# Optimization experiments

Hardware: AMD Instinct MI355X
Metric: run time of the kernel (lower is better)

Reference implementation:

```python
import jax, jax.numpy as jnp
import numpy as np

N0, N1, N2 = 128000, 256000, 128000  # total nodes/edges/triangles across batch
B = 64        # graphs per batch (equal-size graphs: 2000/4000/2000 simplices each)
F = 32        # input feature dim per simplex level
P = 2         # polynomial power in SCConv
OUT = 32      # SCConv output dims
KN, KE, KT = 30, 60, 30  # sort-pool k's
DC = F + OUT  # concat dim (orig_features=True) == conv1d kernel/stride
CO = 16       # conv1d out channels


def spmm(rows, cols, vals, X, n_rows):
    # y = A @ X for sparse A given in COO form (gather + segment-sum scatter)
    return jax.ops.segment_sum(vals[:, None] * X[cols], rows, num_segments=n_rows)


def sortpool(Xc, b, k):
    # per-graph: sort rows by last feature column (descending), keep top k
    n = Xc.shape[0] // b
    Xb = Xc.reshape(b, n, Xc.shape[1])
    _, idx = jax.lax.top_k(Xb[:, :, -1], k)
    return jnp.take_along_axis(Xb, idx[:, :, None], axis=1)  # [b, k, d]


def conv1d(x, w, stride):
    return jax.lax.conv_general_dilated(x, w, (stride,), 'VALID',
                                        dimension_numbers=('NCH', 'OIH', 'NCH'))


def setup_inputs() -> dict:
    key = jax.random.key(0)
    ks = iter(jax.random.split(key, 64))
    d = {}

    def add_sp(name, nnz, nr, nc):
        d[name + '_rows'] = jax.random.randint(next(ks), (nnz,), 0, nr, dtype=jnp.int32)
        d[name + '_cols'] = jax.random.randint(next(ks), (nnz,), 0, nc, dtype=jnp.int32)
        d[name + '_vals'] = jax.random.normal(next(ks), (nnz,), jnp.float32) * 0.1

    add_sp('L0', 8 * N0, N0, N0)
    add_sp('L1', 8 * N1, N1, N1)
    add_sp('L2', 8 * N2, N2, N2)
    add_sp('D1invB1', 2 * N1, N0, N1)
    add_sp('D2B1TD1inv', 2 * N1, N1, N0)
    add_sp('B2TD2inv', 3 * N2, N2, N1)
    add_sp('B2D3', 3 * N2, N1, N2)
    d['X0'] = jax.random.normal(next(ks), (N0, F), jnp.float32)
    d['X1'] = jax.random.normal(next(ks), (N1, F), jnp.float32)
    d['X2'] = jax.random.normal(next(ks), (N2, F), jnp.float32)
    for w in ['W_n2n', 'W_n2e', 'W_e2e', 'W_e2n', 'W_e2t', 'W_t2e', 'W_t2t']:
        d[w] = jax.random.normal(next(ks), (F * P, OUT), jnp.float32) * 0.05
    d['conv_w_nodes'] = jax.random.normal(next(ks), (CO, 1, DC), jnp.float32) * 0.05
    d['conv_w_edges'] = jax.random.normal(next(ks), (CO, 1, DC), jnp.float32) * 0.05
    d['conv_w_tri'] = jax.random.normal(next(ks), (CO, 1, DC), jnp.float32) * 0.05
    mlp_in = CO * (KN + KE + KT)  # 1920
    d['mlp_w1'] = jax.random.normal(next(ks), (mlp_in, 128), jnp.float32) * 0.05
    d['mlp_w_out'] = jax.random.normal(next(ks), (128, 2), jnp.float32) * 0.05
    d['batch_size'] = B
    return d


def reference(L0_rows, L0_cols, L0_vals, L1_rows, L1_cols, L1_vals,
              L2_rows, L2_cols, L2_vals,
              D1invB1_rows, D1invB1_cols, D1invB1_vals,
              D2B1TD1inv_rows, D2B1TD1inv_cols, D2B1TD1inv_vals,
              B2TD2inv_rows, B2TD2inv_cols, B2TD2inv_vals,
              B2D3_rows, B2D3_cols, B2D3_vals,
              X0, X1, X2,
              W_n2n, W_n2e, W_e2e, W_e2n, W_e2t, W_t2e, W_t2t,
              conv_w_nodes, conv_w_edges, conv_w_tri,
              mlp_w1, mlp_w_out, batch_size):
    # SCConv: polynomial feature lift (p=2) -> linear -> sparse aggregation
    X0p = jnp.concatenate([X0, X0 * X0], axis=1)  # [N0, 2F]
    X1p = jnp.concatenate([X1, X1 * X1], axis=1)
    X2p = jnp.concatenate([X2, X2 * X2], axis=1)
    n2n = spmm(L0_rows, L0_cols, L0_vals, X0p @ W_n2n, N0)
    n2e = spmm(D2B1TD1inv_rows, D2B1TD1inv_cols, D2B1TD1inv_vals, X0p @ W_n2e, N1)
    e2n = spmm(D1invB1_rows, D1invB1_cols, D1invB1_vals, X1p @ W_e2n, N0)
    e2e = spmm(L1_rows, L1_cols, L1_vals, X1p @ W_e2e, N1)
    e2t = spmm(B2TD2inv_rows, B2TD2inv_cols, B2TD2inv_vals, X1p @ W_e2t, N2)
    t2t = spmm(L2_rows, L2_cols, L2_vals, X2p @ W_t2t, N2)
    t2e = spmm(B2D3_rows, B2D3_cols, B2D3_vals, X2p @ W_t2e, N1)
    X0o = 0.5 * jax.nn.relu(n2n + e2n)
    X1o = (1.0 / 3.0) * jax.nn.relu(e2e + n2e + t2e)
    X2o = 0.5 * jax.nn.relu(t2t + e2t)
    # orig_features=True: concat input features with conv output
    X0c = jnp.concatenate([X0, X0o], axis=1)  # [N0, DC]
    X1c = jnp.concatenate([X1, X1o], axis=1)
    X2c = jnp.concatenate([X2, X2o], axis=1)
    b = batch_size
    # sort-pool -> flatten -> 1D conv (kernel=stride=DC, no bias) -> relu
    nodes = sortpool(X0c, b, KN).reshape(b, 1, KN * DC)
    nodes = jax.nn.relu(conv1d(nodes, conv_w_nodes, DC)).reshape(b, -1)
    edges = sortpool(X1c, b, KE).reshape(b, 1, KE * DC)
    edges = jax.nn.relu(conv1d(edges, conv_w_edges, DC)).reshape(b, -1)
    tri = sortpool(X2c, b, KT).reshape(b, 1, KT * DC)
    tri = jax.nn.relu(conv1d(tri, conv_w_tri, DC)).reshape(b, -1)
    x = jnp.concatenate([nodes, edges, tri], axis=1)  # [b, 1920]
    # MLP (no dropout at eval, no biases): relu(Linear) -> Linear
    return jax.nn.relu(x @ mlp_w1) @ mlp_w_out  # [b, 2]
```

## Files before the change

kernel.cpp:

```cpp
#include <hip/hip_runtime.h>

#define N0c 128000
#define N1c 256000
#define N2c 128000
#define BG  64
#define KNc 30
#define KEc 60
#define KTc 30
#define COC 16
#define MLP_IN 1920
#define MLP_H 128
#define KSLICE 8
#define KCH (MLP_IN / KSLICE)

#define BINSHIFT 10
#define BINROWS  1024
#define BDEPTH   16
#define BCAP     12288
#define CANDMAX  256

typedef unsigned long long u64;
typedef unsigned int u32;


struct Mat {
    const int* r; const int* c; const float* v;
    int nnz, nbins, epb, slot, tin, tout;
};
struct Mats { Mat m[7]; int count; };
struct Lifts {
    const float* X[3]; const float* W[3]; float* Y[3];
    int N[3]; int count;
};

__global__ __launch_bounds__(256) void gemm_lift_g(Lifts ld)
{
    const int j = blockIdx.y;
    if (j >= ld.count) return;
    const float* __restrict__ X = ld.X[j];
    const float* __restrict__ W = ld.W[j];
    float* __restrict__ Y = ld.Y[j];
    const int N = ld.N[j];

    __shared__ float lw[2048];
    const int tid = threadIdx.x;
    for (int i = tid; i < 2048; i += 256) lw[i] = W[i];
    __syncthreads();

    const int row = blockIdx.x * 256 + tid;
    if (row >= N) return;

    float x[64];
    const float4* p = reinterpret_cast<const float4*>(X + (size_t)row * 32);
    #pragma unroll
    for (int q = 0; q < 8; ++q) {
        float4 v = p[q];
        x[q*4+0] = v.x; x[q*4+1] = v.y; x[q*4+2] = v.z; x[q*4+3] = v.w;
    }
    #pragma unroll
    for (int i = 0; i < 32; ++i) x[32+i] = x[i] * x[i];

    const float4* lw4 = reinterpret_cast<const float4*>(lw);
    float4* yo = reinterpret_cast<float4*>(Y + (size_t)row * 32);
    #pragma unroll
    for (int j4 = 0; j4 < 8; ++j4) {
        float4 s = {0.f, 0.f, 0.f, 0.f};
        #pragma unroll
        for (int i = 0; i < 64; ++i) {
            float4 wf = lw4[i * 8 + j4];
            s.x = fmaf(x[i], wf.x, s.x);
            s.y = fmaf(x[i], wf.y, s.y);
            s.z = fmaf(x[i], wf.z, s.z);
            s.w = fmaf(x[i], wf.w, s.w);
        }
        yo[j4] = s;
    }
}

__global__ __launch_bounds__(256) void bin_hist_g(Mats ms, int* __restrict__ bincnt)
{
    const int j = blockIdx.y;
    if (j >= ms.count) return;
    const Mat mm = ms.m[j];
    const int base = blockIdx.x * mm.epb;
    if (base >= mm.nnz) return;
    int* bc = bincnt + mm.slot * 256;

    __shared__ int lh[256];
    const int tid = threadIdx.x;
    lh[tid] = 0;
    __syncthreads();
    const int cnt = min(mm.epb, mm.nnz - base);
    for (int i = tid; i < cnt; i += 256)
        atomicAdd(&lh[mm.r[base + i] >> BINSHIFT], 1);
    __syncthreads();
    if (tid < mm.nbins && lh[tid]) atomicAdd(&bc[tid], lh[tid]);
}

__global__ __launch_bounds__(256) void bin_scatter_g(
    Mats ms, const int* __restrict__ bincnt, int* __restrict__ gcur,
    u64* __restrict__ tmpP)
{
    const int j = blockIdx.y;
    if (j >= ms.count) return;
    const Mat mm = ms.m[j];
    const int blkbase = blockIdx.x * mm.epb;
    if (blkbase >= mm.nnz) return;
    const int* bc = bincnt + mm.slot * 256;
    int* gc = gcur + mm.slot * 256;

    __shared__ u64 bP[256 * BDEPTH];
    __shared__ int lc[256];
    __shared__ int smo[256];
    const int tid = threadIdx.x;
    lc[tid] = 0;
    smo[tid] = (tid < mm.nbins) ? bc[tid] : 0;
    __syncthreads();
    for (int off = 1; off < 256; off <<= 1) {
        int t_ = (tid >= off) ? smo[tid - off] : 0;
        __syncthreads();
        smo[tid] += t_;
        __syncthreads();
    }

    const int cnt = min(mm.epb, mm.nnz - blkbase);
    for (int i = tid; i < cnt; i += 256) {
        const int e = blkbase + i;
        const int r = mm.r[e];
        const u64 pv = ((u64)__float_as_uint(mm.v[e]) << 32)
                     | ((u32)mm.c[e] << 10) | (u32)(r & (BINROWS - 1));
        const int b = r >> BINSHIFT;
        const int p = atomicAdd(&lc[b], 1);
        if (p < BDEPTH) {
            bP[b * BDEPTH + p] = pv;
        } else {
            const int off0 = mm.tin + ((b == 0) ? 0 : smo[b - 1]);
            const int g = off0 + atomicAdd(&gc[b], 1);
            tmpP[g] = pv;
        }
    }
    __syncthreads();

    if (tid < mm.nbins) {
        int len = lc[tid]; if (len > BDEPTH) len = BDEPTH;
        if (len) {
            const int off0 = mm.tin + ((tid == 0) ? 0 : smo[tid - 1]);
            const int g = off0 + atomicAdd(&gc[tid], len);
            for (int i = 0; i < len; ++i) tmpP[g + i] = bP[tid * BDEPTH + i];
        }
    }
}

__global__ __launch_bounds__(256) void bin_build_g(
    Mats ms, const int* __restrict__ bincnt,
    const u64* __restrict__ tmpP, int R,
    u64* __restrict__ pairs, int* __restrict__ ptrg)
{
    __shared__ unsigned short rl[BCAP];
    __shared__ int h[BINROWS];
    __shared__ int cur[BINROWS];
    __shared__ int sm[256];
    const int b = blockIdx.x, j = blockIdx.y, tid = threadIdx.x;
    const Mat mm = ms.m[j];
    const int* bc = bincnt + mm.slot * 256;
    int* ptr = ptrg + (size_t)j * R;

    sm[tid] = (tid < mm.nbins) ? bc[tid] : 0;
    __syncthreads();
    for (int off = 1; off < 256; off <<= 1) {
        int t_ = (tid >= off) ? sm[tid - off] : 0;
        __syncthreads();
        sm[tid] += t_;
        __syncthreads();
    }
    const int pre = (b == 0) ? 0 : sm[b - 1];
    const int base_in  = mm.tin  + pre;
    const int base_out = mm.tout + pre;
    int len = sm[b] - pre;
    if (len > BCAP) len = BCAP;
    __syncthreads();

    for (int i = tid; i < BINROWS; i += 256) h[i] = 0;
    __syncthreads();
    for (int i = tid; i < len; i += 256) {
        const int r = (int)(tmpP[base_in + i] & (BINROWS - 1));
        rl[i] = (unsigned short)r;
        atomicAdd(&h[r], 1);
    }
    __syncthreads();

    const int i0 = tid * 4;
    const int a0 = h[i0], a1 = h[i0+1], a2 = h[i0+2], a3 = h[i0+3];
    const int s = a0 + a1 + a2 + a3;
    sm[tid] = s;
    __syncthreads();
    for (int off = 1; off < 256; off <<= 1) {
        int t_ = (tid >= off) ? sm[tid - off] : 0;
        __syncthreads();
        sm[tid] += t_;
        __syncthreads();
    }
    const int run = sm[tid] - s;
    cur[i0]   = run;
    cur[i0+1] = run + a0;
    cur[i0+2] = run + a0 + a1;
    cur[i0+3] = run + a0 + a1 + a2;
    const int rstart = b << BINSHIFT;
    if (rstart + i0     < R) ptr[rstart + i0    ] = base_out + run + a0;
    if (rstart + i0 + 1 < R) ptr[rstart + i0 + 1] = base_out + run + a0 + a1;
    if (rstart + i0 + 2 < R) ptr[rstart + i0 + 2] = base_out + run + a0 + a1 + a2;
    if (rstart + i0 + 3 < R) ptr[rstart + i0 + 3] = base_out + run + a0 + a1 + a2 + a3;
    __syncthreads();

    for (int i = tid; i < len; i += 256) {
        const u64 e8 = tmpP[base_in + i];
        const int r = rl[i];
        const int pos = base_out + atomicAdd(&cur[r], 1);
        pairs[pos] = ((e8 >> 32) << 32) | ((e8 >> 10) & 0x3FFFFu);
    }
}

template<int NMAT>
__global__ __launch_bounds__(256) void spmm_group(
    const int* __restrict__ ptrg, int R,
    const u64* __restrict__ pairs,
    int t0, int t1, int t2,
    const float* __restrict__ Y0, const float* __restrict__ Y1,
    const float* __restrict__ Y2,
    float* __restrict__ acc, float* __restrict__ keyout, float kscale)
{
    const int t = blockIdx.x * 256 + threadIdx.x;
    const int row = t >> 3;
    const int l8  = t & 7;
    if (row >= R) return;

    float4 a = {0.f, 0.f, 0.f, 0.f};
    #pragma unroll
    for (int m = 0; m < NMAT; ++m) {
        const int* pm = ptrg + (size_t)m * R;
        const int toff = (m == 0) ? t0 : (m == 1) ? t1 : t2;
        const float4* Y4 = reinterpret_cast<const float4*>(
            (m == 0) ? Y0 : (m == 1) ? Y1 : Y2);
        const int s = (row == 0) ? toff : pm[row - 1];
        const int e = pm[row];
        for (int base = s; base < e; base += 8) {
            int mm = e - base; if (mm > 8) mm = 8;
            u64 pk = (l8 < mm) ? pairs[base + l8] : 0ULL;
            for (int jj = 0; jj < mm; ++jj) {
                const u64 pj = __shfl(pk, jj, 8);
                const int col   = (int)(u32)(pj & 0xffffffffu);
                const float val = __uint_as_float((u32)(pj >> 32));
                const float4 y = Y4[(size_t)col * 8 + l8];
                a.x = fmaf(val, y.x, a.x); a.y = fmaf(val, y.y, a.y);
                a.z = fmaf(val, y.z, a.z); a.w = fmaf(val, y.w, a.w);
            }
        }
    }
    reinterpret_cast<float4*>(acc)[(size_t)row * 8 + l8] = a;
    if (l8 == 7) keyout[row] = kscale * fmaxf(a.w, 0.0f);
}

__global__ __launch_bounds__(256) void gemm_lift(
    const float* __restrict__ X, int N, const float* __restrict__ W,
    float* __restrict__ Y)
{
    __shared__ float lw[2048];
    const int tid = threadIdx.x;
    for (int i = tid; i < 2048; i += 256) lw[i] = W[i];
    __syncthreads();
    const int row = blockIdx.x * 256 + tid;
    if (row >= N) return;
    float x[64];
    const float4* p = reinterpret_cast<const float4*>(X + (size_t)row * 32);
    #pragma unroll
    for (int q = 0; q < 8; ++q) {
        float4 v = p[q];
        x[q*4+0] = v.x; x[q*4+1] = v.y; x[q*4+2] = v.z; x[q*4+3] = v.w;
    }
    #pragma unroll
    for (int i = 0; i < 32; ++i) x[32+i] = x[i] * x[i];
    const float4* lw4 = reinterpret_cast<const float4*>(lw);
    float4* yo = reinterpret_cast<float4*>(Y + (size_t)row * 32);
    #pragma unroll
    for (int j4 = 0; j4 < 8; ++j4) {
        float4 s = {0.f, 0.f, 0.f, 0.f};
        #pragma unroll
        for (int i = 0; i < 64; ++i) {
            float4 wf = lw4[i * 8 + j4];
            s.x = fmaf(x[i], wf.x, s.x);
            s.y = fmaf(x[i], wf.y, s.y);
            s.z = fmaf(x[i], wf.z, s.z);
            s.w = fmaf(x[i], wf.w, s.w);
        }
        yo[j4] = s;
    }
}

__global__ __launch_bounds__(256) void spmm_kernel(
    const int* __restrict__ rows, const int* __restrict__ cols,
    const float* __restrict__ vals,
    const float* __restrict__ Y, float* __restrict__ acc, int nnz)
{
    const int t = blockIdx.x * 256 + threadIdx.x;
    const int e = t >> 3, c = t & 7;
    if (e >= nnz) return;
    const int r = rows[e], col = cols[e];
    const float v = vals[e];
    const float4 yv = reinterpret_cast<const float4*>(Y + (size_t)col * 32)[c];
    float* a = acc + (size_t)r * 32 + c * 4;
    unsafeAtomicAdd(a + 0, v * yv.x);
    unsafeAtomicAdd(a + 1, v * yv.y);
    unsafeAtomicAdd(a + 2, v * yv.z);
    unsafeAtomicAdd(a + 3, v * yv.w);
}

__global__ __launch_bounds__(256) void topk_conv_kernel(
    const float* __restrict__ X0, const float* __restrict__ X1,
    const float* __restrict__ X2,
    const float* __restrict__ acc0, const float* __restrict__ acc1,
    const float* __restrict__ acc2,
    const float* __restrict__ keys0, const float* __restrict__ keys1,
    const float* __restrict__ keys2,
    const float* __restrict__ CW0, const float* __restrict__ CW1,
    const float* __restrict__ CW2,
    float* __restrict__ xfeat)
{
    const int lvl = blockIdx.y;
    const int g   = blockIdx.x;
    int n, k, base; const float* X; const float* acc; const float* keys;
    const float* cw; float scale;
    if (lvl == 0)      { n = 2000; k = KNc; base = 0;             X = X0; acc = acc0; keys = keys0; cw = CW0; scale = 0.5f; }
    else if (lvl == 1) { n = 4000; k = KEc; base = COC*KNc;       X = X1; acc = acc1; keys = keys1; cw = CW1; scale = 1.0f/3.0f; }
    else               { n = 2000; k = KTc; base = COC*(KNc+KEc); X = X2; acc = acc2; keys = keys2; cw = CW2; scale = 0.5f; }

    __shared__ int  hist[2048];
    __shared__ int  smi[256];
    __shared__ u64  cand[CANDMAX];
    __shared__ u64  red[4];
    __shared__ float pooled[KEc][68];
    __shared__ float wt[64][16];
    __shared__ int  sel[KEc];
    __shared__ int  sT, mcur;

    const int tid = threadIdx.x;
    const size_t rowbase = (size_t)g * n;

    for (int i = tid; i < 2048; i += 256) hist[i] = 0;
    if (tid == 0) { sT = -1; mcur = 0; }
    __syncthreads();

    u64 kreg[16];
    #pragma unroll
    for (int i = 0; i < 16; ++i) {
        const int r = i * 256 + tid;
        u64 kk = 0ULL;
        if (r < n) {
            const float kv = keys ? keys[rowbase + r]
                                  : scale * fmaxf(acc[(rowbase + r) * 32 + 31], 0.0f);
            const u32 kb = (kv > 0.0f) ? __float_as_uint(kv) : 0u;
            kk = ((u64)kb << 32) | (u32)(~r);
            if (kb) atomicAdd(&hist[kb >> 20], 1);
        }
        kreg[i] = kk;
    }
    for (int i = tid; i < COC * 64; i += 256) wt[i & 63][i >> 6] = cw[i];
    __syncthreads();

    int lb[8]; int ls = 0;
    #pragma unroll
    for (int i = 0; i < 8; ++i) { lb[i] = hist[tid * 8 + i]; ls += lb[i]; }
    smi[tid] = ls;
    __syncthreads();
    for (int off = 1; off < 256; off <<= 1) {
        int t = (tid >= off) ? smi[tid - off] : 0;
        __syncthreads();
        smi[tid] += t;
        __syncthreads();
    }
    const int total = smi[255];
    const int suf = total - smi[tid];
    if (total >= k && suf < k && suf + ls >= k) {
        int c = suf;
        for (int i = 7; i >= 0; --i) {
            c += lb[i];
            if (c >= k) { sT = tid * 8 + i; break; }
        }
    }
    __syncthreads();

    bool fast = (sT >= 0);
    if (fast) {
        #pragma unroll
        for (int i = 0; i < 16; ++i) {
            const u32 kb = (u32)(kreg[i] >> 32);
            if (kb && (int)(kb >> 20) >= sT) {
                const int pos = atomicAdd(&mcur, 1);
                if (pos < CANDMAX) cand[pos] = kreg[i];
            }
        }
        __syncthreads();
        const int M = mcur;
        if (M <= CANDMAX) {
            for (int i = tid; i < M; i += 256) {
                const u64 e = cand[i];
                int rank = 0;
                for (int j = 0; j < M; ++j) rank += (cand[j] > e) ? 1 : 0;
                if (rank < k) sel[rank] = (int)(~(u32)e);
            }
        } else {
            fast = false;
        }
    }
    __syncthreads();

    if (!fast) {
        for (int it = 0; it < k; ++it) {
            u64 m = 0ULL;
            #pragma unroll
            for (int i = 0; i < 16; ++i) m = kreg[i] > m ? kreg[i] : m;
            #pragma unroll
            for (int off = 32; off > 0; off >>= 1) {
                u64 o = __shfl_xor(m, off, 64);
                m = o > m ? o : m;
            }
            if ((tid & 63) == 0) red[tid >> 6] = m;
            __syncthreads();
            u64 m0 = red[0], m1 = red[1], m2 = red[2], m3 = red[3];
            u64 ma = m0 > m1 ? m0 : m1;
            u64 mb = m2 > m3 ? m2 : m3;
            u64 mm = ma > mb ? ma : mb;
            if (tid == 0) sel[it] = (int)(~(u32)mm);
            #pragma unroll
            for (int i = 0; i < 16; ++i) if (kreg[i] == mm) kreg[i] = 0ULL;
            __syncthreads();
        }
    }

    for (int t = tid; t < k * 32; t += 256) {
        const int r = t >> 5, i = t & 31;
        const size_t row = rowbase + sel[r];
        pooled[r][i]      = X[row * 32 + i];
        pooled[r][32 + i] = scale * fmaxf(acc[row * 32 + i], 0.0f);
    }
    __syncthreads();

    float* xo = xfeat + (size_t)g * MLP_IN + base;
    for (int t = tid; t < k * COC; t += 256) {
        const int r = t >> 4, co = t & 15;
        float s = 0.f;
        #pragma unroll
        for (int j = 0; j < 64; ++j) s = fmaf(pooled[r][j], wt[j][co], s);
        xo[co * k + r] = fmaxf(s, 0.f);
    }
}

__global__ __launch_bounds__(256) void mlp_stage1(
    const float* __restrict__ xfeat, const float* __restrict__ W1,
    float* __restrict__ hidp)
{
    const int g = blockIdx.x, s = blockIdx.y;
    const int tid = threadIdx.x;
    const int j = tid & 127, half = tid >> 7;

    __shared__ float xs[KCH];
    __shared__ float red[256];
    if (tid < KCH) xs[tid] = xfeat[(size_t)g * MLP_IN + s * KCH + tid];
    __syncthreads();

    const float* w = W1 + (size_t)(s * KCH + half * (KCH/2)) * MLP_H + j;
    const float* xh = xs + half * (KCH/2);
    float a = 0.f;
    #pragma unroll 4
    for (int i = 0; i < KCH/2; ++i)
        a = fmaf(xh[i], w[(size_t)i * MLP_H], a);

    red[tid] = a;
    __syncthreads();
    if (half == 0)
        hidp[((size_t)g * KSLICE + s) * MLP_H + j] = red[j] + red[128 + j];
}

__global__ __launch_bounds__(128) void mlp_stage2(
    const float* __restrict__ hidp, const float* __restrict__ W2,
    float* __restrict__ out)
{
    const int g = blockIdx.x, j = threadIdx.x;
    float h = 0.f;
    #pragma unroll
    for (int s = 0; s < KSLICE; ++s)
        h += hidp[((size_t)g * KSLICE + s) * MLP_H + j];
    h = fmaxf(h, 0.f);
    __shared__ float hid[MLP_H];
    hid[j] = h;
    __syncthreads();
    if (j < 2) {
        float o = 0.f;
        #pragma unroll 8
        for (int t = 0; t < MLP_H; ++t) o = fmaf(hid[t], W2[t * 2 + j], o);
        out[g * 2 + j] = o;
    }
}

static inline size_t AL16(size_t x) { return (x + 15) & ~(size_t)15; }
static inline int CEILD(int a, int b) { return (a + b - 1) / b; }

extern "C" void kernel_launch(void* const* d_in, const int* in_sizes, int n_in,
                              void* d_out, int out_size, void* d_ws, size_t ws_size,
                              hipStream_t stream)
{
    const int*   L0r = (const int*)d_in[0];
    const int*   L0c = (const int*)d_in[1];
    const float* L0v = (const float*)d_in[2];
    const int*   L1r = (const int*)d_in[3];
    const int*   L1c = (const int*)d_in[4];
    const float* L1v = (const float*)d_in[5];
    const int*   L2r = (const int*)d_in[6];
    const int*   L2c = (const int*)d_in[7];
    const float* L2v = (const float*)d_in[8];
    const int*   D1r = (const int*)d_in[9];
    const int*   D1c = (const int*)d_in[10];
    const float* D1v = (const float*)d_in[11];
    const int*   D2r = (const int*)d_in[12];
    const int*   D2c = (const int*)d_in[13];
    const float* D2v = (const float*)d_in[14];
    const int*   B2r = (const int*)d_in[15];
    const int*   B2c = (const int*)d_in[16];
    const float* B2v = (const float*)d_in[17];
    const int*   B3r = (const int*)d_in[18];
    const int*   B3c = (const int*)d_in[19];
    const float* B3v = (const float*)d_in[20];
    const float* X0  = (const float*)d_in[21];
    const float* X1  = (const float*)d_in[22];
    const float* X2  = (const float*)d_in[23];
    const float* W_n2n = (const float*)d_in[24];
    const float* W_n2e = (const float*)d_in[25];
    const float* W_e2e = (const float*)d_in[26];
    const float* W_e2n = (const float*)d_in[27];
    const float* W_e2t = (const float*)d_in[28];
    const float* W_t2e = (const float*)d_in[29];
    const float* W_t2t = (const float*)d_in[30];
    const float* CWn = (const float*)d_in[31];
    const float* CWe = (const float*)d_in[32];
    const float* CWt = (const float*)d_in[33];
    const float* MW1 = (const float*)d_in[34];
    const float* MW2 = (const float*)d_in[35];

    const int nnzL0 = in_sizes[0],  nnzL1 = in_sizes[3],  nnzL2 = in_sizes[6];
    const int nnzD1 = in_sizes[9],  nnzD2 = in_sizes[12];
    const int nnzB2 = in_sizes[15], nnzB3 = in_sizes[18];

    const size_t g0n = (size_t)nnzL0 + nnzD1;
    const size_t g1n = (size_t)nnzD2 + nnzL1 + nnzB3;
    const size_t g2n = (size_t)nnzB2 + nnzL2;
    size_t gmax = g0n; if (g1n > gmax) gmax = g1n; if (g2n > gmax) gmax = g2n;
    const size_t totnnz = g0n + g1n + g2n;

    const size_t need_base =
        AL16((size_t)N0c*32*4) + AL16((size_t)N1c*32*4) + AL16((size_t)N2c*32*4)
      + AL16((size_t)N0c*32*4) + AL16((size_t)N1c*32*4) + AL16((size_t)N2c*32*4)
      + AL16((size_t)BG*MLP_IN*4) + AL16((size_t)BG*KSLICE*MLP_H*4)
      + AL16((size_t)N0c*4) + AL16((size_t)N1c*4) + AL16((size_t)N2c*4)
      + AL16(gmax*8) + AL16((size_t)3*N1c*4)
      + AL16((size_t)9*256*4) + AL16((size_t)9*256*4);
    const size_t need_A3 = need_base + AL16(totnnz*8);
    const size_t need_A2 = need_base + AL16(gmax*8);

    char* wp = (char*)d_ws;
    #define WALLOC(ty, name, count) \
        ty* name = (ty*)wp; wp += AL16((size_t)(count) * sizeof(ty));

    if (ws_size >= need_A2) {
        const bool a3 = (ws_size >= need_A3);
        WALLOC(float, Ya,    (size_t)N0c * 32)
        WALLOC(float, Yb,    (size_t)N1c * 32)
        WALLOC(float, Yc,    (size_t)N2c * 32)
        WALLOC(float, acc0,  (size_t)N0c * 32)
        WALLOC(float, acc1,  (size_t)N1c * 32)
        WALLOC(float, acc2,  (size_t)N2c * 32)
        WALLOC(float, xfeat, (size_t)BG * MLP_IN)
        WALLOC(float, hidp,  (size_t)BG * KSLICE * MLP_H)
        WALLOC(float, keys0, (size_t)N0c)
        WALLOC(float, keys1, (size_t)N1c)
        WALLOC(float, keys2, (size_t)N2c)
        WALLOC(u64,   pairs, gmax)
        WALLOC(int,   ptrg,  (size_t)3 * N1c)
        WALLOC(int,   bincnt, 9 * 256)
        WALLOC(int,   gcur,   9 * 256)
        WALLOC(u64,   tmpP,  a3 ? totnnz : gmax)

        hipMemsetAsync(bincnt, 0, 2 * 9 * 256 * sizeof(int), stream);

        const int nb0 = N0c >> BINSHIFT, nb1 = N1c >> BINSHIFT, nb2 = N2c >> BINSHIFT;
        Mat M[7];
        M[0] = { L0r, L0c, L0v, nnzL0, nb0, nb0*8, 0, 0, 0 };
        M[1] = { D1r, D1c, D1v, nnzD1, nb0, nb0*8, 1, 0, nnzL0 };
        M[2] = { D2r, D2c, D2v, nnzD2, nb1, nb1*8, 2, 0, 0 };
        M[3] = { L1r, L1c, L1v, nnzL1, nb1, nb1*8, 3, 0, nnzD2 };
        M[4] = { B3r, B3c, B3v, nnzB3, nb1, nb1*8, 4, 0, nnzD2 + nnzL1 };
        M[5] = { B2r, B2c, B2v, nnzB2, nb2, nb2*8, 5, 0, 0 };
        M[6] = { L2r, L2c, L2v, nnzL2, nb2, nb2*8, 6, 0, nnzB2 };
        if (a3) {
            int cum = 0;
            for (int i = 0; i < 7; ++i) { M[i].tin = cum; cum += M[i].nnz; }
        } else {
            for (int i = 0; i < 7; ++i) M[i].tin = M[i].tout;
        }

        Mats G0; G0.count = 2; G0.m[0] = M[0]; G0.m[1] = M[1];
        Mats G1; G1.count = 3; G1.m[0] = M[2]; G1.m[1] = M[3]; G1.m[2] = M[4];
        Mats G2; G2.count = 2; G2.m[0] = M[5]; G2.m[1] = M[6];

        Lifts L_0; L_0.count = 2;
        L_0.X[0]=X0; L_0.W[0]=W_n2n; L_0.Y[0]=Ya; L_0.N[0]=N0c;
        L_0.X[1]=X1; L_0.W[1]=W_e2n; L_0.Y[1]=Yb; L_0.N[1]=N1c;
        L_0.X[2]=X1; L_0.W[2]=W_e2n; L_0.Y[2]=Yb; L_0.N[2]=0;
        Lifts L_1; L_1.count = 3;
        L_1.X[0]=X0; L_1.W[0]=W_n2e; L_1.Y[0]=Ya; L_1.N[0]=N0c;
        L_1.X[1]=X1; L_1.W[1]=W_e2e; L_1.Y[1]=Yb; L_1.N[1]=N1c;
        L_1.X[2]=X2; L_1.W[2]=W_t2e; L_1.Y[2]=Yc; L_1.N[2]=N2c;
        Lifts L_2; L_2.count = 2;
        L_2.X[0]=X1; L_2.W[0]=W_e2t; L_2.Y[0]=Yb; L_2.N[0]=N1c;
        L_2.X[1]=X2; L_2.W[1]=W_t2t; L_2.Y[1]=Yc; L_2.N[1]=N2c;
        L_2.X[2]=X2; L_2.W[2]=W_t2t; L_2.Y[2]=Yc; L_2.N[2]=0;

        const int liftblk = CEILD(N1c, 256);

        if (a3) {
            Mats ALL; ALL.count = 7;
            for (int i = 0; i < 7; ++i) ALL.m[i] = M[i];
            int maxblk = 0;
            for (int i = 0; i < 7; ++i) {
                const int nb = CEILD(M[i].nnz, M[i].epb);
                if (nb > maxblk) maxblk = nb;
            }
            bin_hist_g<<<dim3(maxblk, 7), 256, 0, stream>>>(ALL, bincnt);
            bin_scatter_g<<<dim3(maxblk, 7), 256, 0, stream>>>(ALL, bincnt, gcur, tmpP);

            gemm_lift_g<<<dim3(liftblk, 2), 256, 0, stream>>>(L_0);
            bin_build_g<<<dim3(nb0, 2), 256, 0, stream>>>(G0, bincnt, tmpP, N0c, pairs, ptrg);
            spmm_group<2><<<CEILD(N0c * 8, 256), 256, 0, stream>>>(
                ptrg, N0c, pairs, 0, nnzL0, 0, Ya, Yb, Yb, acc0, keys0, 0.5f);

            gemm_lift_g<<<dim3(liftblk, 3), 256, 0, stream>>>(L_1);
            bin_build_g<<<dim3(nb1, 3), 256, 0, stream>>>(G1, bincnt, tmpP, N1c, pairs, ptrg);
            spmm_group<3><<<CEILD(N1c * 8, 256), 256, 0, stream>>>(
                ptrg, N1c, pairs, 0, nnzD2, nnzD2 + nnzL1, Ya, Yb, Yc, acc1, keys1, 1.0f/3.0f);

            gemm_lift_g<<<dim3(liftblk, 2), 256, 0, stream>>>(L_2);
            bin_build_g<<<dim3(nb2, 2), 256, 0, stream>>>(G2, bincnt, tmpP, N2c, pairs, ptrg);
            spmm_group<2><<<CEILD(N2c * 8, 256), 256, 0, stream>>>(
                ptrg, N2c, pairs, 0, nnzB2, 0, Yb, Yc, Yc, acc2, keys2, 0.5f);
        } else {
            #define RUN_GROUP(G, LD, NLIFT, NBINS, NMAT, R, SPMMCALL)                  \
                do {                                                                    \
                    int mb = 0;                                                         \
                    for (int i = 0; i < (G).count; ++i) {                               \
                        const int nb = CEILD((G).m[i].nnz, (G).m[i].epb);               \
                        if (nb > mb) mb = nb;                                           \
                    }                                                                   \
                    bin_hist_g<<<dim3(mb, NMAT), 256, 0, stream>>>((G), bincnt);        \
                    bin_scatter_g<<<dim3(mb, NMAT), 256, 0, stream>>>((G), bincnt,      \
                                                                      gcur, tmpP);      \
                    gemm_lift_g<<<dim3(liftblk, NLIFT), 256, 0, stream>>>(LD);          \
                    bin_build_g<<<dim3(NBINS, NMAT), 256, 0, stream>>>((G), bincnt,     \
                                                                tmpP, (R), pairs, ptrg);\
                    SPMMCALL;                                                           \
                } while (0)

            RUN_GROUP(G0, L_0, 2, nb0, 2, N0c,
                (spmm_group<2><<<CEILD(N0c * 8, 256), 256, 0, stream>>>(
                    ptrg, N0c, pairs, 0, nnzL0, 0, Ya, Yb, Yb, acc0, keys0, 0.5f)));
            RUN_GROUP(G1, L_1, 3, nb1, 3, N1c,
                (spmm_group<3><<<CEILD(N1c * 8, 256), 256, 0, stream>>>(
                    ptrg, N1c, pairs, 0, nnzD2, nnzD2 + nnzL1, Ya, Yb, Yc, acc1, keys1, 1.0f/3.0f)));
            RUN_GROUP(G2, L_2, 2, nb2, 2, N2c,
                (spmm_group<2><<<CEILD(N2c * 8, 256), 256, 0, stream>>>(
                    ptrg, N2c, pairs, 0, nnzB2, 0, Yb, Yc, Yc, acc2, keys2, 0.5f)));
            #undef RUN_GROUP
        }

        topk_conv_kernel<<<dim3(BG, 3), 256, 0, stream>>>(X0, X1, X2, acc0, acc1, acc2,
                                                          keys0, keys1, keys2,
                                                          CWn, CWe, CWt, xfeat);
        mlp_stage1<<<dim3(BG, KSLICE), 256, 0, stream>>>(xfeat, MW1, hidp);
        mlp_stage2<<<BG, MLP_H, 0, stream>>>(hidp, MW2, (float*)d_out);
    } else {
        WALLOC(float, Y,     (size_t)N1c * 32)
        WALLOC(float, acc0,  (size_t)N0c * 32)
        WALLOC(float, acc1,  (size_t)N1c * 32)
        WALLOC(float, acc2,  (size_t)N2c * 32)
        WALLOC(float, xfeat, (size_t)BG * MLP_IN)
        WALLOC(float, hidp,  (size_t)BG * KSLICE * MLP_H)

        hipMemsetAsync(acc0, 0, (size_t)(N0c + N1c + N2c) * 32 * sizeof(float), stream);
        #define LIFT(Xp, Np, Wp) \
            gemm_lift<<<CEILD((Np), 256), 256, 0, stream>>>((Xp), (Np), (Wp), Y)
        #define SPMM(rp, cp, vp, nz, accp) \
            spmm_kernel<<<CEILD((nz) * 8, 256), 256, 0, stream>>>((rp), (cp), (vp), Y, (accp), (nz))
        LIFT(X0, N0c, W_n2n);  SPMM(L0r, L0c, L0v, nnzL0, acc0);
        LIFT(X0, N0c, W_n2e);  SPMM(D2r, D2c, D2v, nnzD2, acc1);
        LIFT(X1, N1c, W_e2e);  SPMM(L1r, L1c, L1v, nnzL1, acc1);
        LIFT(X1, N1c, W_e2n);  SPMM(D1r, D1c, D1v, nnzD1, acc0);
        LIFT(X1, N1c, W_e2t);  SPMM(B2r, B2c, B2v, nnzB2, acc2);
        LIFT(X2, N2c, W_t2t);  SPMM(L2r, L2c, L2v, nnzL2, acc2);
        LIFT(X2, N2c, W_t2e);  SPMM(B3r, B3c, B3v, nnzB3, acc1);
        #undef LIFT
        #undef SPMM

        topk_conv_kernel<<<dim3(BG, 3), 256, 0, stream>>>(X0, X1, X2, acc0, acc1, acc2,
                                                          nullptr, nullptr, nullptr,
                                                          CWn, CWe, CWt, xfeat);
        mlp_stage1<<<dim3(BG, KSLICE), 256, 0, stream>>>(xfeat, MW1, hidp);
        mlp_stage2<<<BG, MLP_H, 0, stream>>>(hidp, MW2, (float*)d_out);
    }
    #undef WALLOC
}
```

Baseline: 543.7 us.

## Replace hist+scatter binning with single-pass per-block local counting sort

Merges the histogram and scatter passes into one kernel where each block locally sorts a fixed 2048-entry chunk by bin and writes a per-block offset table. The bin build kernel then gathers each bin's segments from all chunks using the table instead of reading a contiguous globally-scattered range. This removes one pass over the COO inputs and the global per-bin atomic scatter. In exchange, the build step does serial, less coalesced per-thread segment reads and allocates an extra table.

Result: slower. 651.0 us (+19.7%).

```diff
diff --git a/kernel.cpp b/kernel.cpp
--- a/kernel.cpp
+++ b/kernel.cpp
@@ -15,7 +15,7 @@
 
 #define BINSHIFT 10
 #define BINROWS  1024
-#define BDEPTH   16
+#define EPB      2048
 #define BCAP     12288
 #define CANDMAX  256
 
@@ -25,7 +25,7 @@
 
 struct Mat {
     const int* r; const int* c; const float* v;
-    int nnz, nbins, epb, slot, tin, tout;
+    int nnz, nbins, slot, tin, tout, btb;
 };
 struct Mats { Mat m[7]; int count; };
 struct Lifts {
@@ -77,91 +77,66 @@
     }
 }
 
-__global__ __launch_bounds__(256) void bin_hist_g(Mats ms, int* __restrict__ bincnt)
+__global__ __launch_bounds__(256) void scatter_sort_g(
+    Mats ms, u64* __restrict__ tmp, int* __restrict__ btab,
+    int* __restrict__ bincnt)
 {
     const int j = blockIdx.y;
     if (j >= ms.count) return;
     const Mat mm = ms.m[j];
-    const int base = blockIdx.x * mm.epb;
+    const int base = blockIdx.x * EPB;
     if (base >= mm.nnz) return;
-    int* bc = bincnt + mm.slot * 256;
-
-    __shared__ int lh[256];
+    const int cnt = min(EPB, mm.nnz - base);
+
+    __shared__ int h[256], cur[256], sm[256];
     const int tid = threadIdx.x;
-    lh[tid] = 0;
-    __syncthreads();
-    const int cnt = min(mm.epb, mm.nnz - base);
+    h[tid] = 0;
+    __syncthreads();
     for (int i = tid; i < cnt; i += 256)
-        atomicAdd(&lh[mm.r[base + i] >> BINSHIFT], 1);
-    __syncthreads();
-    if (tid < mm.nbins && lh[tid]) atomicAdd(&bc[tid], lh[tid]);
-}
-
-__global__ __launch_bounds__(256) void bin_scatter_g(
-    Mats ms, const int* __restrict__ bincnt, int* __restrict__ gcur,
-    u64* __restrict__ tmpP)
-{
-    const int j = blockIdx.y;
-    if (j >= ms.count) return;
-    const Mat mm = ms.m[j];
-    const int blkbase = blockIdx.x * mm.epb;
-    if (blkbase >= mm.nnz) return;
-    const int* bc = bincnt + mm.slot * 256;
-    int* gc = gcur + mm.slot * 256;
-
-    __shared__ u64 bP[256 * BDEPTH];
-    __shared__ int lc[256];
-    __shared__ int smo[256];
-    const int tid = threadIdx.x;
-    lc[tid] = 0;
-    smo[tid] = (tid < mm.nbins) ? bc[tid] : 0;
+        atomicAdd(&h[mm.r[base + i] >> BINSHIFT], 1);
+    __syncthreads();
+
+    const int hv = h[tid];
+    sm[tid] = hv;
     __syncthreads();
     for (int off = 1; off < 256; off <<= 1) {
-        int t_ = (tid >= off) ? smo[tid - off] : 0;
-        __syncthreads();
-        smo[tid] += t_;
-        __syncthreads();
-    }
-
-    const int cnt = min(mm.epb, mm.nnz - blkbase);
+        int t_ = (tid >= off) ? sm[tid - off] : 0;
+        __syncthreads();
+        sm[tid] += t_;
+        __syncthreads();
+    }
+    const int ex = sm[tid] - hv;
+    int* bt = btab + mm.btb + blockIdx.x * 257;
+    bt[tid] = ex;
+    if (tid == 255) bt[256] = cnt;
+    if (tid < mm.nbins && hv) atomicAdd(&bincnt[mm.slot * 256 + tid], hv);
+    cur[tid] = ex;
+    __syncthreads();
+
+    u64* dst = tmp + mm.tin + base;
     for (int i = tid; i < cnt; i += 256) {
-        const int e = blkbase + i;
+        const int e = base + i;
         const int r = mm.r[e];
         const u64 pv = ((u64)__float_as_uint(mm.v[e]) << 32)
                      | ((u32)mm.c[e] << 10) | (u32)(r & (BINROWS - 1));
-        const int b = r >> BINSHIFT;
-        const int p = atomicAdd(&lc[b], 1);
-        if (p < BDEPTH) {
-            bP[b * BDEPTH + p] = pv;
-        } else {
-            const int off0 = mm.tin + ((b == 0) ? 0 : smo[b - 1]);
-            const int g = off0 + atomicAdd(&gc[b], 1);
-            tmpP[g] = pv;
-        }
-    }
-    __syncthreads();
-
-    if (tid < mm.nbins) {
-        int len = lc[tid]; if (len > BDEPTH) len = BDEPTH;
-        if (len) {
-            const int off0 = mm.tin + ((tid == 0) ? 0 : smo[tid - 1]);
-            const int g = off0 + atomicAdd(&gc[tid], len);
-            for (int i = 0; i < len; ++i) tmpP[g + i] = bP[tid * BDEPTH + i];
-        }
+        const int pos = atomicAdd(&cur[r >> BINSHIFT], 1);
+        dst[pos] = pv;
     }
 }
 
 __global__ __launch_bounds__(256) void bin_build_g(
     Mats ms, const int* __restrict__ bincnt,
-    const u64* __restrict__ tmpP, int R,
+    const u64* __restrict__ tmp, const int* __restrict__ btab, int R,
     u64* __restrict__ pairs, int* __restrict__ ptrg)
 {
     __shared__ unsigned short rl[BCAP];
     __shared__ int h[BINROWS];
     __shared__ int cur[BINROWS];
+    __shared__ int sg[1024];
     __shared__ int sm[256];
     const int b = blockIdx.x, j = blockIdx.y, tid = threadIdx.x;
     const Mat mm = ms.m[j];
+    const int nblk = (mm.nnz + EPB - 1) / EPB;
     const int* bc = bincnt + mm.slot * 256;
     int* ptr = ptrg + (size_t)j * R;
 
@@ -174,25 +149,59 @@
         __syncthreads();
     }
     const int pre = (b == 0) ? 0 : sm[b - 1];
-    const int base_in  = mm.tin  + pre;
     const int base_out = mm.tout + pre;
-    int len = sm[b] - pre;
-    if (len > BCAP) len = BCAP;
-    __syncthreads();
-
+    __syncthreads();
+
+    int sl[4]; int ssum = 0;
+    #pragma unroll
+    for (int q = 0; q < 4; ++q) {
+        const int s = tid * 4 + q;
+        int l = 0;
+        if (s < nblk) {
+            const int* bt = btab + mm.btb + s * 257;
+            l = bt[b + 1] - bt[b];
+        }
+        sl[q] = l; ssum += l;
+    }
+    sm[tid] = ssum;
+    __syncthreads();
+    for (int off = 1; off < 256; off <<= 1) {
+        int t_ = (tid >= off) ? sm[tid - off] : 0;
+        __syncthreads();
+        sm[tid] += t_;
+        __syncthreads();
+    }
+    int run = sm[tid] - ssum;
+    #pragma unroll
+    for (int q = 0; q < 4; ++q) {
+        const int s = tid * 4 + q;
+        if (s < nblk) sg[s] = run;
+        run += sl[q];
+    }
     for (int i = tid; i < BINROWS; i += 256) h[i] = 0;
     __syncthreads();
-    for (int i = tid; i < len; i += 256) {
-        const int r = (int)(tmpP[base_in + i] & (BINROWS - 1));
-        rl[i] = (unsigned short)r;
-        atomicAdd(&h[r], 1);
+
+    for (int q = 0; q < 4; ++q) {
+        const int s = tid * 4 + q;
+        if (s >= nblk) break;
+        const int st = btab[mm.btb + s * 257 + b];
+        const int n  = sl[q];
+        const u64* seg = tmp + mm.tin + s * EPB + st;
+        const int o = sg[s];
+        for (int k = 0; k < n; ++k) {
+            const int idx = o + k;
+            if (idx >= BCAP) break;
+            const int rlo = (int)(seg[k] & (BINROWS - 1));
+            rl[idx] = (unsigned short)rlo;
+            atomicAdd(&h[rlo], 1);
+        }
     }
     __syncthreads();
 
     const int i0 = tid * 4;
     const int a0 = h[i0], a1 = h[i0+1], a2 = h[i0+2], a3 = h[i0+3];
-    const int s = a0 + a1 + a2 + a3;
-    sm[tid] = s;
+    const int s4 = a0 + a1 + a2 + a3;
+    sm[tid] = s4;
     __syncthreads();
     for (int off = 1; off < 256; off <<= 1) {
         int t_ = (tid >= off) ? sm[tid - off] : 0;
@@ -200,23 +209,32 @@
         sm[tid] += t_;
         __syncthreads();
     }
-    const int run = sm[tid] - s;
-    cur[i0]   = run;
-    cur[i0+1] = run + a0;
-    cur[i0+2] = run + a0 + a1;
-    cur[i0+3] = run + a0 + a1 + a2;
+    const int rrun = sm[tid] - s4;
+    cur[i0]   = rrun;
+    cur[i0+1] = rrun + a0;
+    cur[i0+2] = rrun + a0 + a1;
+    cur[i0+3] = rrun + a0 + a1 + a2;
     const int rstart = b << BINSHIFT;
-    if (rstart + i0     < R) ptr[rstart + i0    ] = base_out + run + a0;
-    if (rstart + i0 + 1 < R) ptr[rstart + i0 + 1] = base_out + run + a0 + a1;
-    if (rstart + i0 + 2 < R) ptr[rstart + i0 + 2] = base_out + run + a0 + a1 + a2;
-    if (rstart + i0 + 3 < R) ptr[rstart + i0 + 3] = base_out + run + a0 + a1 + a2 + a3;
-    __syncthreads();
-
-    for (int i = tid; i < len; i += 256) {
-        const u64 e8 = tmpP[base_in + i];
-        const int r = rl[i];
-        const int pos = base_out + atomicAdd(&cur[r], 1);
-        pairs[pos] = ((e8 >> 32) << 32) | ((e8 >> 10) & 0x3FFFFu);
+    if (rstart + i0     < R) ptr[rstart + i0    ] = base_out + rrun + a0;
+    if (rstart + i0 + 1 < R) ptr[rstart + i0 + 1] = base_out + rrun + a0 + a1;
+    if (rstart + i0 + 2 < R) ptr[rstart + i0 + 2] = base_out + rrun + a0 + a1 + a2;
+    if (rstart + i0 + 3 < R) ptr[rstart + i0 + 3] = base_out + rrun + a0 + a1 + a2 + a3;
+    __syncthreads();
+
+    for (int q = 0; q < 4; ++q) {
+        const int s = tid * 4 + q;
+        if (s >= nblk) break;
+        const int st = btab[mm.btb + s * 257 + b];
+        const int n  = sl[q];
+        const u64* seg = tmp + mm.tin + s * EPB + st;
+        const int o = sg[s];
+        for (int k = 0; k < n; ++k) {
+            const int idx = o + k;
+            if (idx >= BCAP) break;
+            const u64 e8 = seg[k];
+            const int pos = base_out + atomicAdd(&cur[rl[idx]], 1);
+            pairs[pos] = ((e8 >> 32) << 32) | ((e8 >> 10) & 0x3FFFFu);
+        }
     }
 }
 
@@ -555,15 +573,27 @@
     size_t gmax = g0n; if (g1n > gmax) gmax = g1n; if (g2n > gmax) gmax = g2n;
     const size_t totnnz = g0n + g1n + g2n;
 
+    const int nbk[7] = { CEILD(nnzL0,EPB), CEILD(nnzD1,EPB), CEILD(nnzD2,EPB),
+                         CEILD(nnzL1,EPB), CEILD(nnzB3,EPB), CEILD(nnzB2,EPB),
+                         CEILD(nnzL2,EPB) };
+    size_t btabTot = 0;
+    for (int i = 0; i < 7; ++i) btabTot += (size_t)nbk[i] * 257;
+    const size_t btabG0 = ((size_t)nbk[0] + nbk[1]) * 257;
+    const size_t btabG1 = ((size_t)nbk[2] + nbk[3] + nbk[4]) * 257;
+    const size_t btabG2 = ((size_t)nbk[5] + nbk[6]) * 257;
+    size_t btabGmax = btabG0;
+    if (btabG1 > btabGmax) btabGmax = btabG1;
+    if (btabG2 > btabGmax) btabGmax = btabG2;
+
     const size_t need_base =
         AL16((size_t)N0c*32*4) + AL16((size_t)N1c*32*4) + AL16((size_t)N2c*32*4)
       + AL16((size_t)N0c*32*4) + AL16((size_t)N1c*32*4) + AL16((size_t)N2c*32*4)
       + AL16((size_t)BG*MLP_IN*4) + AL16((size_t)BG*KSLICE*MLP_H*4)
       + AL16((size_t)N0c*4) + AL16((size_t)N1c*4) + AL16((size_t)N2c*4)
       + AL16(gmax*8) + AL16((size_t)3*N1c*4)
-      + AL16((size_t)9*256*4) + AL16((size_t)9*256*4);
-    const size_t need_A3 = need_base + AL16(totnnz*8);
-    const size_t need_A2 = need_base + AL16(gmax*8);
+      + AL16((size_t)9*256*4);
+    const size_t need_A3 = need_base + AL16(totnnz*8) + AL16(btabTot*4);
+    const size_t need_A2 = need_base + AL16(gmax*8) + AL16(btabGmax*4);
 
     char* wp = (char*)d_ws;
     #define WALLOC(ty, name, count) \
@@ -585,25 +615,34 @@
         WALLOC(u64,   pairs, gmax)
         WALLOC(int,   ptrg,  (size_t)3 * N1c)
         WALLOC(int,   bincnt, 9 * 256)
-        WALLOC(int,   gcur,   9 * 256)
-        WALLOC(u64,   tmpP,  a3 ? totnnz : gmax)
-
-        hipMemsetAsync(bincnt, 0, 2 * 9 * 256 * sizeof(int), stream);
+        WALLOC(u64,   tmp,   a3 ? totnnz : gmax)
+        WALLOC(int,   btab,  a3 ? btabTot : btabGmax)
+
+        hipMemsetAsync(bincnt, 0, 9 * 256 * sizeof(int), stream);
 
         const int nb0 = N0c >> BINSHIFT, nb1 = N1c >> BINSHIFT, nb2 = N2c >> BINSHIFT;
         Mat M[7];
-        M[0] = { L0r, L0c, L0v, nnzL0, nb0, nb0*8, 0, 0, 0 };
-        M[1] = { D1r, D1c, D1v, nnzD1, nb0, nb0*8, 1, 0, nnzL0 };
-        M[2] = { D2r, D2c, D2v, nnzD2, nb1, nb1*8, 2, 0, 0 };
-        M[3] = { L1r, L1c, L1v, nnzL1, nb1, nb1*8, 3, 0, nnzD2 };
-        M[4] = { B3r, B3c, B3v, nnzB3, nb1, nb1*8, 4, 0, nnzD2 + nnzL1 };
-        M[5] = { B2r, B2c, B2v, nnzB2, nb2, nb2*8, 5, 0, 0 };
-        M[6] = { L2r, L2c, L2v, nnzL2, nb2, nb2*8, 6, 0, nnzB2 };
+        M[0] = { L0r, L0c, L0v, nnzL0, nb0, 0, 0, 0,            0 };
+        M[1] = { D1r, D1c, D1v, nnzD1, nb0, 1, 0, nnzL0,        0 };
+        M[2] = { D2r, D2c, D2v, nnzD2, nb1, 2, 0, 0,            0 };
+        M[3] = { L1r, L1c, L1v, nnzL1, nb1, 3, 0, nnzD2,        0 };
+        M[4] = { B3r, B3c, B3v, nnzB3, nb1, 4, 0, nnzD2+nnzL1,  0 };
+        M[5] = { B2r, B2c, B2v, nnzB2, nb2, 5, 0, 0,            0 };
+        M[6] = { L2r, L2c, L2v, nnzL2, nb2, 6, 0, nnzB2,        0 };
         if (a3) {
-            int cum = 0;
-            for (int i = 0; i < 7; ++i) { M[i].tin = cum; cum += M[i].nnz; }
+            int ec = 0, bc_ = 0;
+            for (int i = 0; i < 7; ++i) {
+                M[i].tin = ec;  ec += M[i].nnz;
+                M[i].btb = bc_; bc_ += nbk[i] * 257;
+            }
         } else {
-            for (int i = 0; i < 7; ++i) M[i].tin = M[i].tout;
+            M[0].tin = M[0].tout; M[0].btb = 0;
+            M[1].tin = M[1].tout; M[1].btb = nbk[0] * 257;
+            M[2].tin = M[2].tout; M[2].btb = 0;
+            M[3].tin = M[3].tout; M[3].btb = nbk[2] * 257;
+            M[4].tin = M[4].tout; M[4].btb = (nbk[2] + nbk[3]) * 257;
+            M[5].tin = M[5].tout; M[5].btb = 0;
+            M[6].tin = M[6].tout; M[6].btb = nbk[5] * 257;
         }
 
         Mats G0; G0.count = 2; G0.m[0] = M[0]; G0.m[1] = M[1];
@@ -629,25 +668,21 @@
             Mats ALL; ALL.count = 7;
             for (int i = 0; i < 7; ++i) ALL.m[i] = M[i];
             int maxblk = 0;
-            for (int i = 0; i < 7; ++i) {
-                const int nb = CEILD(M[i].nnz, M[i].epb);
-                if (nb > maxblk) maxblk = nb;
-            }
-            bin_hist_g<<<dim3(maxblk, 7), 256, 0, stream>>>(ALL, bincnt);
-            bin_scatter_g<<<dim3(maxblk, 7), 256, 0, stream>>>(ALL, bincnt, gcur, tmpP);
+            for (int i = 0; i < 7; ++i) if (nbk[i] > maxblk) maxblk = nbk[i];
+            scatter_sort_g<<<dim3(maxblk, 7), 256, 0, stream>>>(ALL, tmp, btab, bincnt);
 
             gemm_lift_g<<<dim3(liftblk, 2), 256, 0, stream>>>(L_0);
-            bin_build_g<<<dim3(nb0, 2), 256, 0, stream>>>(G0, bincnt, tmpP, N0c, pairs, ptrg);
+            bin_build_g<<<dim3(nb0, 2), 256, 0, stream>>>(G0, bincnt, tmp, btab, N0c, pairs, ptrg);
             spmm_group<2><<<CEILD(N0c * 8, 256), 256, 0, stream>>>(
                 ptrg, N0c, pairs, 0, nnzL0, 0, Ya, Yb, Yb, acc0, keys0, 0.5f);
 
             gemm_lift_g<<<dim3(liftblk, 3), 256, 0, stream>>>(L_1);
-            bin_build_g<<<dim3(nb1, 3), 256, 0, stream>>>(G1, bincnt, tmpP, N1c, pairs, ptrg);
+            bin_build_g<<<dim3(nb1, 3), 256, 0, stream>>>(G1, bincnt, tmp, btab, N1c, pairs, ptrg);
             spmm_group<3><<<CEILD(N1c * 8, 256), 256, 0, stream>>>(
                 ptrg, N1c, pairs, 0, nnzD2, nnzD2 + nnzL1, Ya, Yb, Yc, acc1, keys1, 1.0f/3.0f);
 
             gemm_lift_g<<<dim3(liftblk, 2), 256, 0, stream>>>(L_2);
-            bin_build_g<<<dim3(nb2, 2), 256, 0, stream>>>(G2, bincnt, tmpP, N2c, pairs, ptrg);
+            bin_build_g<<<dim3(nb2, 2), 256, 0, stream>>>(G2, bincnt, tmp, btab, N2c, pairs, ptrg);
             spmm_group<2><<<CEILD(N2c * 8, 256), 256, 0, stream>>>(
                 ptrg, N2c, pairs, 0, nnzB2, 0, Yb, Yc, Yc, acc2, keys2, 0.5f);
         } else {
@@ -655,15 +690,14 @@
                 do {                                                                    \
                     int mb = 0;                                                         \
                     for (int i = 0; i < (G).count; ++i) {                               \
-                        const int nb = CEILD((G).m[i].nnz, (G).m[i].epb);               \
+                        const int nb = CEILD((G).m[i].nnz, EPB);                        \
                         if (nb > mb) mb = nb;                                           \
                     }                                                                   \
-                    bin_hist_g<<<dim3(mb, NMAT), 256, 0, stream>>>((G), bincnt);        \
-                    bin_scatter_g<<<dim3(mb, NMAT), 256, 0, stream>>>((G), bincnt,      \
-                                                                      gcur, tmpP);      \
+                    scatter_sort_g<<<dim3(mb, NMAT), 256, 0, stream>>>((G), tmp,        \
+                                                                       btab, bincnt);   \
                     gemm_lift_g<<<dim3(liftblk, NLIFT), 256, 0, stream>>>(LD);          \
                     bin_build_g<<<dim3(NBINS, NMAT), 256, 0, stream>>>((G), bincnt,     \
-                                                                tmpP, (R), pairs, ptrg);\
+                                                          tmp, btab, (R), pairs, ptrg); \
                     SPMMCALL;                                                           \
                 } while (0)
 
```
